# Performance work log

Hardware: AMD Instinct MI355X
Metric: run time of the kernel (lower is better)

Reference implementation:

```python
import jax, jax.numpy as jnp
import numpy as np

Nw, Nt, IN_DIM, OUT_DIM, H, FEAT = 200000, 20000, 128, 256, 8, 64
DH = OUT_DIM // H
DEG = 32
E = Nt * DEG
FFN = 512
NEG_SLOPE = 0.01  # F.leaky_relu default


def setup_inputs() -> dict:
    key = jax.random.key(0)
    ks = jax.random.split(key, 12)
    w = jax.random.normal(ks[0], (Nw, IN_DIM), jnp.float32)
    t = jax.random.normal(ks[1], (Nt, OUT_DIM), jnp.float32)
    topic_feat = jax.random.normal(ks[2], (Nt, FEAT), jnp.float32)
    edge_src = jax.random.randint(ks[3], (E,), 0, Nw)
    # every topic node gets exactly DEG in-edges (sorted dst, no empty segments)
    edge_dst = jnp.repeat(jnp.arange(Nt), DEG)
    s = lambda k, sh, f: jax.random.normal(k, sh, jnp.float32) * np.float32(f)
    fc_w = s(ks[4], (H, IN_DIM, DH), 1.0 / np.sqrt(IN_DIM))
    attn_a = s(ks[5], (H, 2 * DH), 1.0 / np.sqrt(2 * DH))
    dstfeat_w = s(ks[6], (H, FEAT, DH), 1.0 / np.sqrt(FEAT))
    proj_w = s(ks[7], (2 * OUT_DIM, OUT_DIM), 1.0 / np.sqrt(2 * OUT_DIM))
    proj_b = jnp.zeros((OUT_DIM,), jnp.float32)
    ffn_w1 = s(ks[8], (OUT_DIM, FFN), 1.0 / np.sqrt(OUT_DIM))
    ffn_b1 = jnp.zeros((FFN,), jnp.float32)
    ffn_w2 = s(ks[9], (FFN, OUT_DIM), 1.0 / np.sqrt(FFN))
    ffn_b2 = jnp.zeros((OUT_DIM,), jnp.float32)
    ln_scale = jnp.ones((OUT_DIM,), jnp.float32)
    ln_bias = jnp.zeros((OUT_DIM,), jnp.float32)
    return dict(w=w, t=t, topic_feat=topic_feat, edge_src=edge_src, edge_dst=edge_dst,
                fc_w=fc_w, attn_a=attn_a, dstfeat_w=dstfeat_w, proj_w=proj_w, proj_b=proj_b,
                ffn_w1=ffn_w1, ffn_b1=ffn_b1, ffn_w2=ffn_w2, ffn_b2=ffn_b2,
                ln_scale=ln_scale, ln_bias=ln_bias)


def reference(w, t, topic_feat, edge_src, edge_dst, fc_w, attn_a, dstfeat_w,
              proj_w, proj_b, ffn_w1, ffn_b1, ffn_w2, ffn_b2, ln_scale, ln_bias):
    # per-head projections: z on word (src) nodes, dstfeat on topic (dst) nodes
    z = jnp.einsum('ni,hid->hnd', w, fc_w)              # [H, Nw, DH]
    dz = jnp.einsum('nf,hfd->hnd', topic_feat, dstfeat_w)  # [H, Nt, DH]
    # attn_fc(cat(z_src, dstfeat)) decomposes into per-node dot products
    s_src = jnp.einsum('hnd,hd->hn', z, attn_a[:, :DH])   # [H, Nw]
    s_dst = jnp.einsum('hnd,hd->hn', dz, attn_a[:, DH:])  # [H, Nt]
    e = s_src[:, edge_src] + s_dst[:, edge_dst]           # [H, E]
    e = jnp.where(e >= 0, e, NEG_SLOPE * e)               # leaky_relu
    # segment softmax over incoming edges of each dst node (DGL mailbox softmax)
    seg_max = jax.vmap(lambda v: jax.ops.segment_max(v, edge_dst, num_segments=Nt))(e)
    seg_max = jnp.where(jnp.isfinite(seg_max), seg_max, 0.0)  # guard empty segments
    p = jnp.exp(e - seg_max[:, edge_dst])
    denom = jax.vmap(lambda v: jax.ops.segment_sum(v, edge_dst, num_segments=Nt))(p)
    alpha = p / jnp.maximum(denom[:, edge_dst], 1e-9)     # [H, E]
    msg = alpha[:, :, None] * z[:, edge_src, :]           # [H, E, DH]
    agg = jax.vmap(lambda m: jax.ops.segment_sum(m, edge_dst, num_segments=Nt))(msg)  # [H, Nt, DH]
    h = jnp.transpose(agg, (1, 0, 2)).reshape(Nt, OUT_DIM)  # head concat
    h = jax.nn.elu(h)
    h = jnp.concatenate([h, t], axis=-1) @ proj_w + proj_b  # [Nt, OUT_DIM]
    # PositionwiseFeedForward: LN -> gelu -> linear -> residual (dropout off in eval)
    mu = jnp.mean(h, axis=-1, keepdims=True)
    var = jnp.var(h, axis=-1, keepdims=True)
    xn = (h - mu) / jnp.sqrt(var + 1e-6) * ln_scale + ln_bias
    inter = jax.nn.gelu(xn @ ffn_w1 + ffn_b1, approximate=False)
    return (inter @ ffn_w2 + ffn_b2) + h
```

## Files before the change

### kernel.cpp

```cpp
#include <hip/hip_runtime.h>
#include <hip/hip_bf16.h>

typedef __attribute__((ext_vector_type(8))) short short8v;
typedef __attribute__((ext_vector_type(4))) float f32x4;

#define NW 200000
#define NT 20000
#define KIN 128
#define ODIM 256
#define NH 8
#define DH_ 32
#define FEAT_ 64
#define DEG_ 32
#define FFN_ 512

#define WS_Z     0ull
#define WS_SSRC  102400000ull
#define WS_SDST  108800000ull
#define WS_HBF   109440000ull
#define WS_TBF   119680000ull
#define WS_B1T   129920000ull
#define WS_PWT   129985536ull
#define WS_W1T   130247680ull
#define WS_W2T   130509824ull
#define WS_ABT   130771968ull


__device__ __forceinline__ unsigned short f2bf(float x) {
    __hip_bfloat16 b = __float2bfloat16(x);
    return *reinterpret_cast<unsigned short*>(&b);
}
__device__ __forceinline__ float bf2f(unsigned short u) {
    unsigned int v = ((unsigned int)u) << 16;
    return __uint_as_float(v);
}

__global__ __launch_bounds__(256) void prep_w(const float* __restrict__ fc_w,
        const float* __restrict__ proj_w, const float* __restrict__ w1,
        const float* __restrict__ w2, const float* __restrict__ attn_a,
        unsigned short* __restrict__ b1f, unsigned short* __restrict__ pwf,
        unsigned short* __restrict__ w1f, unsigned short* __restrict__ w2f,
        unsigned short* __restrict__ abt) {
    int i = blockIdx.x * 256 + threadIdx.x;
    int j = i & 7, l = (i >> 3) & 63;
    int l16 = l & 15, lq = l >> 4;
    if (i < 32768) {
        int kk = (i >> 9) & 3, g = i >> 11;
        int c = g * 16 + l16, k = kk * 32 + lq * 8 + j;
        int h = c >> 5, d = c & 31;
        b1f[i] = f2bf(fc_w[(h * KIN + k) * DH_ + d]);
    }
    if (i < 4096) {
        int h = i >> 8, p = i & 255;
        int c = (p >> 6) * 64 + (p & 3) * 16 + ((p >> 2) & 15);
        abt[i] = ((c >> 5) == h) ? f2bf(attn_a[h * 64 + (c & 31)]) : (unsigned short)0;
    }
    {
        int kk = (i >> 9) & 15, g = i >> 13;
        int c = g * 16 + l16, k = kk * 32 + lq * 8 + j;
        int kp = k;
        if (k < 256)
            kp = ((k >> 6) << 6) + (k & 3) * 16 + ((k >> 2) & 15);
        pwf[i] = f2bf(proj_w[(size_t)kp * ODIM + c]);
    }
    {
        int kk = (i >> 9) & 7, g = i >> 12;
        int c = g * 16 + l16, k = kk * 32 + lq * 8 + j;
        w1f[i] = f2bf(w1[(size_t)k * FFN_ + c]);
    }
    {
        int kk = (i >> 9) & 15, g = i >> 13;
        int c = g * 16 + l16, k = kk * 32 + lq * 8 + j;
        w2f[i] = f2bf(w2[(size_t)k * ODIM + c]);
    }
}

__global__ __launch_bounds__(256) void prep_t(const float* __restrict__ t,
                                              unsigned short* __restrict__ tbf) {
    int i = blockIdx.x * 256 + threadIdx.x;
    const float4* p = (const float4*)(t + (size_t)i * 8);
    float4 a = p[0], b = p[1];
    short8v o;
    o[0] = (short)f2bf(a.x); o[1] = (short)f2bf(a.y);
    o[2] = (short)f2bf(a.z); o[3] = (short)f2bf(a.w);
    o[4] = (short)f2bf(b.x); o[5] = (short)f2bf(b.y);
    o[6] = (short)f2bf(b.z); o[7] = (short)f2bf(b.w);
    *((short8v*)tbf + i) = o;
}

#define ZRP 264
#define TPB 5
__global__ __launch_bounds__(256) void k1_z(const float* __restrict__ w,
        const unsigned short* __restrict__ b1f, const unsigned short* __restrict__ abt,
        unsigned short* __restrict__ z, float* __restrict__ s_src) {
    __shared__ unsigned short aS[2][64 * 136];
    __shared__ unsigned short zR[64 * ZRP];
    const int tid = threadIdx.x;
    const int wv = tid >> 6, l = tid & 63;
    const int l16 = l & 15, lq = l >> 4;
    const int tile0 = blockIdx.x * TPB;
    float4 vb[8];
    #pragma unroll
    for (int j = 0; j < 8; ++j) {
        int i = tid + j * 256;
        int r = i >> 5, kq = i & 31;
        vb[j] = *(const float4*)(w + (size_t)(tile0 * 64 + r) * KIN + kq * 4);
    }
    #pragma unroll
    for (int j = 0; j < 8; ++j) {
        int i = tid + j * 256;
        int r = i >> 5, kq = i & 31;
        ushort4 u;
        u.x = f2bf(vb[j].x); u.y = f2bf(vb[j].y);
        u.z = f2bf(vb[j].z); u.w = f2bf(vb[j].w);
        *(ushort4*)(&aS[0][r * 136 + kq * 4]) = u;
    }
    for (int t = 0; t < TPB; ++t) {
        const int cur = t & 1;
        const int row0 = (tile0 + t) * 64;
        if (t < TPB - 1) {
            #pragma unroll
            for (int j = 0; j < 8; ++j) {
                int i = tid + j * 256;
                int r = i >> 5, kq = i & 31;
                vb[j] = *(const float4*)(w + (size_t)(row0 + 64 + r) * KIN + kq * 4);
            }
        }
        __syncthreads();
        f32x4 acc[4][4];
        #pragma unroll
        for (int a = 0; a < 4; ++a)
            #pragma unroll
            for (int b = 0; b < 4; ++b)
                acc[a][b] = (f32x4){0.f, 0.f, 0.f, 0.f};
        #pragma unroll
        for (int kk = 0; kk < 4; ++kk) {
            short8v af[4], bfr[4];
            #pragma unroll
            for (int rf = 0; rf < 4; ++rf)
                af[rf] = *(const short8v*)(&aS[cur][(rf * 16 + l16) * 136 + kk * 32 + lq * 8]);
            #pragma unroll
            for (int cf = 0; cf < 4; ++cf)
                bfr[cf] = *(const short8v*)((const short*)b1f +
                            ((((wv * 4 + cf) * 4 + kk) << 9) + l * 8));
            #pragma unroll
            for (int rf = 0; rf < 4; ++rf)
                #pragma unroll
                for (int cf = 0; cf < 4; ++cf)
                    acc[rf][cf] = __builtin_amdgcn_mfma_f32_16x16x32_bf16(
                        af[rf], bfr[cf], acc[rf][cf], 0, 0, 0);
        }
        #pragma unroll
        for (int rl = 0; rl < 4; ++rl)
            #pragma unroll
            for (int q = 0; q < 4; ++q) {
                int row = rl * 16 + lq * 4 + q;
                ushort4 u;
                u.x = f2bf(acc[rl][0][q]); u.y = f2bf(acc[rl][1][q]);
                u.z = f2bf(acc[rl][2][q]); u.w = f2bf(acc[rl][3][q]);
                *(ushort4*)(&zR[row * ZRP + wv * 64 + l16 * 4]) = u;
            }
        __syncthreads();
        {
            const int base = wv * 16;
            f32x4 sacc = (f32x4){0.f, 0.f, 0.f, 0.f};
            #pragma unroll
            for (int kk = 0; kk < 8; ++kk) {
                short8v a = *(const short8v*)(&zR[(base + l16) * ZRP + kk * 32 + lq * 8]);
                short8v b = *(const short8v*)((const short*)abt + (size_t)l16 * 256 + kk * 32 + lq * 8);
                sacc = __builtin_amdgcn_mfma_f32_16x16x32_bf16(a, b, sacc, 0, 0, 0);
            }
            if (l16 < NH) {
                #pragma unroll
                for (int q = 0; q < 4; ++q)
                    s_src[(size_t)(row0 + base + lq * 4 + q) * NH + l16] = sacc[q];
            }
        }
        #pragma unroll
        for (int j = 0; j < 8; ++j) {
            int idx = tid + j * 256;
            int r = idx >> 5, ch = idx & 31;
            short8v v = *(const short8v*)(&zR[r * ZRP + ch * 8]);
            *(short8v*)(z + (size_t)(row0 + r) * ODIM + ch * 8) = v;
        }
        if (t < TPB - 1) {
            #pragma unroll
            for (int j = 0; j < 8; ++j) {
                int i = tid + j * 256;
                int r = i >> 5, kq = i & 31;
                ushort4 u;
                u.x = f2bf(vb[j].x); u.y = f2bf(vb[j].y);
                u.z = f2bf(vb[j].z); u.w = f2bf(vb[j].w);
                *(ushort4*)(&aS[cur ^ 1][r * 136 + kq * 4]) = u;
            }
        }
    }
}

__global__ __launch_bounds__(256) void k_sdst(const float* __restrict__ topic_feat,
        const float* __restrict__ dstfeat_w, const float* __restrict__ attn_a,
        float* __restrict__ s_dst) {
    __shared__ float rS[NH * 65];
    __shared__ float tfS[32 * 65];
    const int tid = threadIdx.x;
    for (int i = tid; i < NH * FEAT_; i += 256) {
        int h = i >> 6, f = i & 63;
        const float* dw = dstfeat_w + (size_t)(h * FEAT_ + f) * DH_;
        const float* aa = attn_a + h * 64 + DH_;
        float s = 0.f;
        #pragma unroll
        for (int d = 0; d < DH_; ++d) s += dw[d] * aa[d];
        rS[h * 65 + f] = s;
    }
    const int n0 = blockIdx.x * 32;
    for (int i = tid; i < 32 * FEAT_; i += 256) {
        int n = i >> 6, f = i & 63;
        tfS[n * 65 + f] = topic_feat[(size_t)(n0 + n) * FEAT_ + f];
    }
    __syncthreads();
    int n = tid >> 3, h = tid & 7;
    float s = 0.f;
    #pragma unroll
    for (int f = 0; f < FEAT_; ++f) s += tfS[n * 65 + f] * rS[h * 65 + f];
    s_dst[(size_t)(n0 + n) * NH + h] = s;
}

__global__ __launch_bounds__(256) void k2_attn(const int* __restrict__ edge_src,
        const float* __restrict__ s_src, const float* __restrict__ s_dst,
        const unsigned short* __restrict__ z, unsigned short* __restrict__ hbf) {
    __shared__ int srcS[4][32];
    __shared__ float aS[4][32][8];
    const int tid = threadIdx.x;
    const int nd = tid >> 6, l = tid & 63;
    const int n = blockIdx.x * 4 + nd;
    if (l < 32) srcS[nd][l] = edge_src[(size_t)n * DEG_ + l];
    __syncthreads();
    {
        int e = l & 31, h0 = (l >> 5) * 4;
        int s = srcS[nd][e];
        float4 ss = *(const float4*)(s_src + (size_t)s * NH + h0);
        float4 sd = *(const float4*)(s_dst + (size_t)n * NH + h0);
        float v[4] = {ss.x + sd.x, ss.y + sd.y, ss.z + sd.z, ss.w + sd.w};
        #pragma unroll
        for (int j = 0; j < 4; ++j) v[j] = (v[j] >= 0.f) ? v[j] : 0.01f * v[j];
        float al[4];
        #pragma unroll
        for (int j = 0; j < 4; ++j) {
            float m = v[j];
            #pragma unroll
            for (int off = 16; off >= 1; off >>= 1)
                m = fmaxf(m, __shfl_xor(m, off));
            float p = expf(v[j] - m);
            float su = p;
            #pragma unroll
            for (int off = 16; off >= 1; off >>= 1)
                su += __shfl_xor(su, off);
            al[j] = p / fmaxf(su, 1e-9f);
        }
        float4 a4 = {al[0], al[1], al[2], al[3]};
        *(float4*)(&aS[nd][e][h0]) = a4;
    }
    __syncthreads();
    {
        const int half = l >> 5, cl = l & 31;
        const int h0 = (cl >> 3) * 2;
        float acc[8];
        #pragma unroll
        for (int j = 0; j < 8; ++j) acc[j] = 0.f;
        #pragma unroll 4
        for (int ee = 0; ee < 16; ++ee) {
            int e = ee * 2 + half;
            int sp = srcS[nd][e];
            float a_lo = aS[nd][e][h0], a_hi = aS[nd][e][h0 + 1];
            short8v zv = *(const short8v*)(z + (size_t)sp * ODIM + cl * 8);
            #pragma unroll
            for (int u = 0; u < 8; ++u) {
                float a = ((u >> 1) & 1) ? a_hi : a_lo;
                acc[u] += a * bf2f((unsigned short)zv[u]);
            }
        }
        #pragma unroll
        for (int j = 0; j < 8; ++j)
            acc[j] += __shfl_xor(acc[j], 32);
        if (half == 0) {
            short8v o;
            #pragma unroll
            for (int j = 0; j < 8; ++j) {
                float v = (acc[j] > 0.f) ? acc[j] : expm1f(acc[j]);
                o[j] = (short)f2bf(v);
            }
            *(short8v*)(hbf + (size_t)n * ODIM + cl * 8) = o;
        }
    }
}

#define BUFP 524
#define XNP  268
__global__ __launch_bounds__(256, 3) void k34_ffn(const unsigned short* __restrict__ hbf,
        const unsigned short* __restrict__ tbf, const unsigned short* __restrict__ pwf,
        const float* __restrict__ proj_b, const float* __restrict__ ln_scale,
        const float* __restrict__ ln_bias, const unsigned short* __restrict__ w1f,
        const float* __restrict__ b1, const unsigned short* __restrict__ w2f,
        const float* __restrict__ b2, float* __restrict__ out) {
    __shared__ unsigned short buf[32 * BUFP];
    __shared__ unsigned short xnS[32 * XNP];
    __shared__ float lnP[4][32], lnQ[4][32];
    __shared__ float muS[32], rsS[32];
    const int tid = threadIdx.x;
    const int row0 = blockIdx.x * 32;
    #pragma unroll
    for (int j = 0; j < 8; ++j) {
        int i = tid + j * 256;
        int r = i >> 6, cq = i & 63;
        ushort4 hv = *(const ushort4*)(hbf + (size_t)(row0 + r) * ODIM + cq * 4);
        *(ushort4*)(&buf[r * BUFP + cq * 4]) = hv;
        ushort4 tv = *(const ushort4*)(tbf + (size_t)(row0 + r) * ODIM + cq * 4);
        *(ushort4*)(&buf[r * BUFP + 256 + cq * 4]) = tv;
    }
    __syncthreads();
    const int wv = tid >> 6, l = tid & 63;
    const int l16 = l & 15, lq = l >> 4;
    const int l8 = l * 8;
    f32x4 acc0[2][4];
    #pragma unroll
    for (int rf = 0; rf < 2; ++rf)
        #pragma unroll
        for (int cf = 0; cf < 4; ++cf) acc0[rf][cf] = (f32x4){0.f, 0.f, 0.f, 0.f};
    {
        short8v bp[2][4];
        #pragma unroll
        for (int cf = 0; cf < 4; ++cf)
            bp[0][cf] = *(const short8v*)((const short*)pwf + ((((wv * 4 + cf) * 16) << 9) + l8));
        #pragma unroll
        for (int kk = 0; kk < 16; ++kk) {
            const int cur = kk & 1;
            if (kk < 15) {
                #pragma unroll
                for (int cf = 0; cf < 4; ++cf)
                    bp[cur ^ 1][cf] = *(const short8v*)((const short*)pwf +
                        ((((wv * 4 + cf) * 16 + kk + 1) << 9) + l8));
            }
            short8v a0 = *(const short8v*)(&buf[l16 * BUFP + kk * 32 + lq * 8]);
            short8v a1 = *(const short8v*)(&buf[(16 + l16) * BUFP + kk * 32 + lq * 8]);
            #pragma unroll
            for (int cf = 0; cf < 4; ++cf) {
                acc0[0][cf] = __builtin_amdgcn_mfma_f32_16x16x32_bf16(a0, bp[cur][cf], acc0[0][cf], 0, 0, 0);
                acc0[1][cf] = __builtin_amdgcn_mfma_f32_16x16x32_bf16(a1, bp[cur][cf], acc0[1][cf], 0, 0, 0);
            }
        }
    }
    #pragma unroll
    for (int cf = 0; cf < 4; ++cf) {
        float bb = proj_b[wv * 64 + cf * 16 + l16];
        #pragma unroll
        for (int rf = 0; rf < 2; ++rf)
            #pragma unroll
            for (int q = 0; q < 4; ++q) acc0[rf][cf][q] += bb;
    }
    #pragma unroll
    for (int rf = 0; rf < 2; ++rf)
        #pragma unroll
        for (int q = 0; q < 4; ++q) {
            float s = 0.f, s2 = 0.f;
            #pragma unroll
            for (int cf = 0; cf < 4; ++cf) {
                float v = acc0[rf][cf][q];
                s += v; s2 += v * v;
            }
            s  += __shfl_xor(s, 1);  s2 += __shfl_xor(s2, 1);
            s  += __shfl_xor(s, 2);  s2 += __shfl_xor(s2, 2);
            s  += __shfl_xor(s, 4);  s2 += __shfl_xor(s2, 4);
            s  += __shfl_xor(s, 8);  s2 += __shfl_xor(s2, 8);
            if (l16 == 0) {
                int row = rf * 16 + lq * 4 + q;
                lnP[wv][row] = s; lnQ[wv][row] = s2;
            }
        }
    __syncthreads();
    if (tid < 32) {
        float s = lnP[0][tid] + lnP[1][tid] + lnP[2][tid] + lnP[3][tid];
        float s2 = lnQ[0][tid] + lnQ[1][tid] + lnQ[2][tid] + lnQ[3][tid];
        float mu = s * (1.f / 256.f);
        float var = s2 * (1.f / 256.f) - mu * mu;
        muS[tid] = mu;
        rsS[tid] = rsqrtf(var + 1e-6f);
    }
    __syncthreads();
    #pragma unroll
    for (int cf = 0; cf < 4; ++cf) {
        int c = wv * 64 + cf * 16 + l16;
        float ls = ln_scale[c], lb = ln_bias[c];
        #pragma unroll
        for (int rf = 0; rf < 2; ++rf)
            #pragma unroll
            for (int q = 0; q < 4; ++q) {
                int row = rf * 16 + lq * 4 + q;
                float x = (acc0[rf][cf][q] - muS[row]) * rsS[row] * ls + lb;
                xnS[row * XNP + c] = f2bf(x);
            }
    }
    __syncthreads();
    {
        f32x4 acc1[2][8];
        #pragma unroll
        for (int rf = 0; rf < 2; ++rf)
            #pragma unroll
            for (int cf = 0; cf < 8; ++cf) acc1[rf][cf] = (f32x4){0.f, 0.f, 0.f, 0.f};
        #pragma unroll 2
        for (int kk = 0; kk < 8; ++kk) {
            short8v a0 = *(const short8v*)(&xnS[l16 * XNP + kk * 32 + lq * 8]);
            short8v a1 = *(const short8v*)(&xnS[(16 + l16) * XNP + kk * 32 + lq * 8]);
            #pragma unroll
            for (int cf = 0; cf < 8; ++cf) {
                short8v b = *(const short8v*)((const short*)w1f +
                    ((((wv * 8 + cf) * 8 + kk) << 9) + l8));
                acc1[0][cf] = __builtin_amdgcn_mfma_f32_16x16x32_bf16(a0, b, acc1[0][cf], 0, 0, 0);
                acc1[1][cf] = __builtin_amdgcn_mfma_f32_16x16x32_bf16(a1, b, acc1[1][cf], 0, 0, 0);
            }
        }
        #pragma unroll
        for (int cf = 0; cf < 8; ++cf) {
            int c = wv * 128 + cf * 16 + l16;
            float bb = b1[c];
            #pragma unroll
            for (int rf = 0; rf < 2; ++rf)
                #pragma unroll
                for (int q = 0; q < 4; ++q) {
                    float x = acc1[rf][cf][q] + bb;
                    x = 0.5f * x * (1.f + erff(x * 0.70710678118654752f));
                    buf[(rf * 16 + lq * 4 + q) * BUFP + c] = f2bf(x);
                }
        }
    }
    __syncthreads();
    {
        f32x4 acc2[2][4];
        #pragma unroll
        for (int rf = 0; rf < 2; ++rf)
            #pragma unroll
            for (int cf = 0; cf < 4; ++cf) acc2[rf][cf] = (f32x4){0.f, 0.f, 0.f, 0.f};
        short8v bp[2][4];
        #pragma unroll
        for (int cf = 0; cf < 4; ++cf)
            bp[0][cf] = *(const short8v*)((const short*)w2f + ((((wv * 4 + cf) * 16) << 9) + l8));
        #pragma unroll
        for (int kk = 0; kk < 16; ++kk) {
            const int cur = kk & 1;
            if (kk < 15) {
                #pragma unroll
                for (int cf = 0; cf < 4; ++cf)
                    bp[cur ^ 1][cf] = *(const short8v*)((const short*)w2f +
                        ((((wv * 4 + cf) * 16 + kk + 1) << 9) + l8));
            }
            short8v a0 = *(const short8v*)(&buf[l16 * BUFP + kk * 32 + lq * 8]);
            short8v a1 = *(const short8v*)(&buf[(16 + l16) * BUFP + kk * 32 + lq * 8]);
            #pragma unroll
            for (int cf = 0; cf < 4; ++cf) {
                acc2[0][cf] = __builtin_amdgcn_mfma_f32_16x16x32_bf16(a0, bp[cur][cf], acc2[0][cf], 0, 0, 0);
                acc2[1][cf] = __builtin_amdgcn_mfma_f32_16x16x32_bf16(a1, bp[cur][cf], acc2[1][cf], 0, 0, 0);
            }
        }
        #pragma unroll
        for (int cf = 0; cf < 4; ++cf) {
            int c = wv * 64 + cf * 16 + l16;
            float bb = b2[c];
            #pragma unroll
            for (int rf = 0; rf < 2; ++rf)
                #pragma unroll
                for (int q = 0; q < 4; ++q) {
                    int row = rf * 16 + lq * 4 + q;
                    out[(size_t)(row0 + row) * ODIM + c] =
                        acc2[rf][cf][q] + bb + acc0[rf][cf][q];
                }
        }
    }
}

extern "C" void kernel_launch(void* const* d_in, const int* in_sizes, int n_in,
                              void* d_out, int out_size, void* d_ws, size_t ws_size,
                              hipStream_t stream) {
    const float* w          = (const float*)d_in[0];
    const float* t          = (const float*)d_in[1];
    const float* topic_feat = (const float*)d_in[2];
    const int*   edge_src   = (const int*)d_in[3];
    const float* fc_w       = (const float*)d_in[5];
    const float* attn_a     = (const float*)d_in[6];
    const float* dstfeat_w  = (const float*)d_in[7];
    const float* proj_w     = (const float*)d_in[8];
    const float* proj_b     = (const float*)d_in[9];
    const float* ffn_w1     = (const float*)d_in[10];
    const float* ffn_b1     = (const float*)d_in[11];
    const float* ffn_w2     = (const float*)d_in[12];
    const float* ffn_b2     = (const float*)d_in[13];
    const float* ln_scale   = (const float*)d_in[14];
    const float* ln_bias    = (const float*)d_in[15];
    float* out = (float*)d_out;

    char* ws = (char*)d_ws;
    unsigned short* z    = (unsigned short*)(ws + WS_Z);
    float* s_src         = (float*)(ws + WS_SSRC);
    float* s_dst         = (float*)(ws + WS_SDST);
    unsigned short* hbf  = (unsigned short*)(ws + WS_HBF);
    unsigned short* tbf  = (unsigned short*)(ws + WS_TBF);
    unsigned short* b1f  = (unsigned short*)(ws + WS_B1T);
    unsigned short* pwf  = (unsigned short*)(ws + WS_PWT);
    unsigned short* w1f  = (unsigned short*)(ws + WS_W1T);
    unsigned short* w2f  = (unsigned short*)(ws + WS_W2T);
    unsigned short* abt  = (unsigned short*)(ws + WS_ABT);

    hipLaunchKernelGGL(prep_w, dim3(512),           dim3(256), 0, stream,
                       fc_w, proj_w, ffn_w1, ffn_w2, attn_a, b1f, pwf, w1f, w2f, abt);
    hipLaunchKernelGGL(prep_t, dim3(2500),          dim3(256), 0, stream, t, tbf);
    hipLaunchKernelGGL(k1_z,   dim3(NW / (64*TPB)), dim3(256), 0, stream,
                       w, b1f, abt, z, s_src);
    hipLaunchKernelGGL(k_sdst, dim3(NT / 32),       dim3(256), 0, stream,
                       topic_feat, dstfeat_w, attn_a, s_dst);
    hipLaunchKernelGGL(k2_attn, dim3(NT / 4),       dim3(256), 0, stream,
                       edge_src, s_src, s_dst, z, hbf);
    hipLaunchKernelGGL(k34_ffn, dim3(NT / 32),      dim3(256), 0, stream,
                       hbf, tbf, pwf, proj_b, ln_scale, ln_bias,
                       w1f, ffn_b1, w2f, ffn_b2, out);
}
```

Measured before the change: 181.5 us.

## Fuse attention aggregation kernel into FFN kernel, keep h in LDS

Merges the edge-softmax/aggregation kernel into the projection+FFN kernel so each block computes its 32 rows of ELU-aggregated h directly into shared memory, removing the hbf global round trip and one launch. Each wave processes 8 destination nodes serially, using xnS as scratch for alpha and shuffles for source indices. In exchange, the gather phase now runs with only 625 blocks at limited occupancy (launch bounds 3), so the latency-bound z gathers get less parallelism than the previous 5000-block kernel had.

```diff
diff --git a/kernel.cpp b/kernel.cpp
--- a/kernel.cpp
+++ b/kernel.cpp
@@ -17,7 +17,6 @@
 #define WS_Z     0ull
 #define WS_SSRC  102400000ull
 #define WS_SDST  108800000ull
-#define WS_HBF   109440000ull
 #define WS_TBF   119680000ull
 #define WS_B1T   129920000ull
 #define WS_PWT   129985536ull
@@ -225,102 +224,104 @@
     s_dst[(size_t)(n0 + n) * NH + h] = s;
 }
 
-__global__ __launch_bounds__(256) void k2_attn(const int* __restrict__ edge_src,
-        const float* __restrict__ s_src, const float* __restrict__ s_dst,
-        const unsigned short* __restrict__ z, unsigned short* __restrict__ hbf) {
-    __shared__ int srcS[4][32];
-    __shared__ float aS[4][32][8];
-    const int tid = threadIdx.x;
-    const int nd = tid >> 6, l = tid & 63;
-    const int n = blockIdx.x * 4 + nd;
-    if (l < 32) srcS[nd][l] = edge_src[(size_t)n * DEG_ + l];
-    __syncthreads();
-    {
-        int e = l & 31, h0 = (l >> 5) * 4;
-        int s = srcS[nd][e];
-        float4 ss = *(const float4*)(s_src + (size_t)s * NH + h0);
-        float4 sd = *(const float4*)(s_dst + (size_t)n * NH + h0);
-        float v[4] = {ss.x + sd.x, ss.y + sd.y, ss.z + sd.z, ss.w + sd.w};
-        #pragma unroll
-        for (int j = 0; j < 4; ++j) v[j] = (v[j] >= 0.f) ? v[j] : 0.01f * v[j];
-        float al[4];
-        #pragma unroll
-        for (int j = 0; j < 4; ++j) {
-            float m = v[j];
-            #pragma unroll
-            for (int off = 16; off >= 1; off >>= 1)
-                m = fmaxf(m, __shfl_xor(m, off));
-            float p = expf(v[j] - m);
-            float su = p;
-            #pragma unroll
-            for (int off = 16; off >= 1; off >>= 1)
-                su += __shfl_xor(su, off);
-            al[j] = p / fmaxf(su, 1e-9f);
-        }
-        float4 a4 = {al[0], al[1], al[2], al[3]};
-        *(float4*)(&aS[nd][e][h0]) = a4;
-    }
-    __syncthreads();
-    {
-        const int half = l >> 5, cl = l & 31;
-        const int h0 = (cl >> 3) * 2;
-        float acc[8];
-        #pragma unroll
-        for (int j = 0; j < 8; ++j) acc[j] = 0.f;
-        #pragma unroll 4
-        for (int ee = 0; ee < 16; ++ee) {
-            int e = ee * 2 + half;
-            int sp = srcS[nd][e];
-            float a_lo = aS[nd][e][h0], a_hi = aS[nd][e][h0 + 1];
-            short8v zv = *(const short8v*)(z + (size_t)sp * ODIM + cl * 8);
-            #pragma unroll
-            for (int u = 0; u < 8; ++u) {
-                float a = ((u >> 1) & 1) ? a_hi : a_lo;
-                acc[u] += a * bf2f((unsigned short)zv[u]);
-            }
-        }
-        #pragma unroll
-        for (int j = 0; j < 8; ++j)
-            acc[j] += __shfl_xor(acc[j], 32);
-        if (half == 0) {
-            short8v o;
-            #pragma unroll
-            for (int j = 0; j < 8; ++j) {
-                float v = (acc[j] > 0.f) ? acc[j] : expm1f(acc[j]);
-                o[j] = (short)f2bf(v);
-            }
-            *(short8v*)(hbf + (size_t)n * ODIM + cl * 8) = o;
-        }
-    }
-}
-
 #define BUFP 524
 #define XNP  268
-__global__ __launch_bounds__(256, 3) void k34_ffn(const unsigned short* __restrict__ hbf,
-        const unsigned short* __restrict__ tbf, const unsigned short* __restrict__ pwf,
-        const float* __restrict__ proj_b, const float* __restrict__ ln_scale,
-        const float* __restrict__ ln_bias, const unsigned short* __restrict__ w1f,
-        const float* __restrict__ b1, const unsigned short* __restrict__ w2f,
-        const float* __restrict__ b2, float* __restrict__ out) {
-    __shared__ unsigned short buf[32 * BUFP];
-    __shared__ unsigned short xnS[32 * XNP];
+__global__ __launch_bounds__(256, 3) void k234(const int* __restrict__ edge_src,
+        const float* __restrict__ s_src, const float* __restrict__ s_dst,
+        const unsigned short* __restrict__ z, const unsigned short* __restrict__ tbf,
+        const unsigned short* __restrict__ pwf, const float* __restrict__ proj_b,
+        const float* __restrict__ ln_scale, const float* __restrict__ ln_bias,
+        const unsigned short* __restrict__ w1f, const float* __restrict__ b1,
+        const unsigned short* __restrict__ w2f, const float* __restrict__ b2,
+        float* __restrict__ out) {
+    __shared__ __align__(16) unsigned short buf[32 * BUFP];
+    __shared__ __align__(16) unsigned short xnS[32 * XNP];
     __shared__ float lnP[4][32], lnQ[4][32];
     __shared__ float muS[32], rsS[32];
     const int tid = threadIdx.x;
     const int row0 = blockIdx.x * 32;
+    const int wv = tid >> 6, l = tid & 63;
+    const int l16 = l & 15, lq = l >> 4;
+    const int l8 = l * 8;
     #pragma unroll
     for (int j = 0; j < 8; ++j) {
         int i = tid + j * 256;
         int r = i >> 6, cq = i & 63;
-        ushort4 hv = *(const ushort4*)(hbf + (size_t)(row0 + r) * ODIM + cq * 4);
-        *(ushort4*)(&buf[r * BUFP + cq * 4]) = hv;
         ushort4 tv = *(const ushort4*)(tbf + (size_t)(row0 + r) * ODIM + cq * 4);
         *(ushort4*)(&buf[r * BUFP + 256 + cq * 4]) = tv;
     }
+    {
+        float* alphaW = (float*)xnS + wv * 256;
+        for (int nd = 0; nd < 8; ++nd) {
+            const int r = wv * 8 + nd;
+            const int n = row0 + r;
+            int srcv = edge_src[(size_t)n * DEG_ + (l & 31)];
+            {
+                int h0 = (l >> 5) * 4;
+                float4 ss = *(const float4*)(s_src + (size_t)srcv * NH + h0);
+                float4 sd = *(const float4*)(s_dst + (size_t)n * NH + h0);
+                float v[4] = {ss.x + sd.x, ss.y + sd.y, ss.z + sd.z, ss.w + sd.w};
+                #pragma unroll
+                for (int j = 0; j < 4; ++j) v[j] = (v[j] >= 0.f) ? v[j] : 0.01f * v[j];
+                float al[4];
+                #pragma unroll
+                for (int j = 0; j < 4; ++j) {
+                    float m = v[j];
+                    #pragma unroll
+                    for (int off = 16; off >= 1; off >>= 1)
+                        m = fmaxf(m, __shfl_xor(m, off));
+                    float p = expf(v[j] - m);
+                    float su = p;
+                    #pragma unroll
+                    for (int off = 16; off >= 1; off >>= 1)
+                        su += __shfl_xor(su, off);
+                    al[j] = p / fmaxf(su, 1e-9f);
+                }
+                float4 a4 = {al[0], al[1], al[2], al[3]};
+                *(float4*)(&alphaW[(l & 31) * 8 + h0]) = a4;
+            }
+            asm volatile("s_waitcnt lgkmcnt(0)" ::: "memory");
+            {
+                const int half = l >> 5, cl = l & 31;
+                const int h0a = (cl >> 3) * 2;
+                float acc[8];
+                #pragma unroll
+                for (int j = 0; j < 8; ++j) acc[j] = 0.f;
+                #pragma unroll 4
+                for (int ee = 0; ee < 16; ++ee) {
+                    int e = ee * 2 + half;
+                    int sp = __shfl(srcv, e);
+                    float a_lo = alphaW[e * 8 + h0a];
+                    float a_hi = alphaW[e * 8 + h0a + 1];
+                    short8v zv = *(const short8v*)(z + (size_t)sp * ODIM + cl * 8);
+                    #pragma unroll
+                    for (int u = 0; u < 8; ++u) {
+                        float a = ((u >> 1) & 1) ? a_hi : a_lo;
+                        acc[u] += a * bf2f((unsigned short)zv[u]);
+                    }
+                }
+                #pragma unroll
+                for (int j = 0; j < 8; ++j)
+                    acc[j] += __shfl_xor(acc[j], 32);
+                if (half == 0) {
+                    ushort4 o0, o1;
+                    float v0 = (acc[0] > 0.f) ? acc[0] : expm1f(acc[0]);
+                    float v1 = (acc[1] > 0.f) ? acc[1] : expm1f(acc[1]);
+                    float v2 = (acc[2] > 0.f) ? acc[2] : expm1f(acc[2]);
+                    float v3 = (acc[3] > 0.f) ? acc[3] : expm1f(acc[3]);
+                    float v4 = (acc[4] > 0.f) ? acc[4] : expm1f(acc[4]);
+                    float v5 = (acc[5] > 0.f) ? acc[5] : expm1f(acc[5]);
+                    float v6 = (acc[6] > 0.f) ? acc[6] : expm1f(acc[6]);
+                    float v7 = (acc[7] > 0.f) ? acc[7] : expm1f(acc[7]);
+                    o0.x = f2bf(v0); o0.y = f2bf(v1); o0.z = f2bf(v2); o0.w = f2bf(v3);
+                    o1.x = f2bf(v4); o1.y = f2bf(v5); o1.z = f2bf(v6); o1.w = f2bf(v7);
+                    *(ushort4*)(&buf[r * BUFP + cl * 8]) = o0;
+                    *(ushort4*)(&buf[r * BUFP + cl * 8 + 4]) = o1;
+                }
+            }
+        }
+    }
     __syncthreads();
-    const int wv = tid >> 6, l = tid & 63;
-    const int l16 = l & 15, lq = l >> 4;
-    const int l8 = l * 8;
     f32x4 acc0[2][4];
     #pragma unroll
     for (int rf = 0; rf < 2; ++rf)
@@ -500,7 +501,6 @@
     unsigned short* z    = (unsigned short*)(ws + WS_Z);
     float* s_src         = (float*)(ws + WS_SSRC);
     float* s_dst         = (float*)(ws + WS_SDST);
-    unsigned short* hbf  = (unsigned short*)(ws + WS_HBF);
     unsigned short* tbf  = (unsigned short*)(ws + WS_TBF);
     unsigned short* b1f  = (unsigned short*)(ws + WS_B1T);
     unsigned short* pwf  = (unsigned short*)(ws + WS_PWT);
@@ -515,9 +515,7 @@
                        w, b1f, abt, z, s_src);
     hipLaunchKernelGGL(k_sdst, dim3(NT / 32),       dim3(256), 0, stream,
                        topic_feat, dstfeat_w, attn_a, s_dst);
-    hipLaunchKernelGGL(k2_attn, dim3(NT / 4),       dim3(256), 0, stream,
-                       edge_src, s_src, s_dst, z, hbf);
-    hipLaunchKernelGGL(k34_ffn, dim3(NT / 32),      dim3(256), 0, stream,
-                       hbf, tbf, pwf, proj_b, ln_scale, ln_bias,
-                       w1f, ffn_b1, w2f, ffn_b2, out);
-}
+    hipLaunchKernelGGL(k234,   dim3(NT / 32),       dim3(256), 0, stream,
+                       edge_src, s_src, s_dst, z, tbf, pwf, proj_b,
+                       ln_scale, ln_bias, w1f, ffn_b1, w2f, ffn_b2, out);
+}
```

New measurement: 171.3 us, median of 2. 5.6% less time.
